# Optimization experiments

Measured on AMD Instinct MI355X. Metric: run time of the kernel, lower is better.

Reference implementation:

```python
import jax, jax.numpy as jnp
import numpy as np

N = 4096
IN_DIM = 512
NUM_HEADS = 8
SUB_DIM = 64
ETA = 0.5
LAMBDA_SPARSE = 0.1
EDGE_PROB = 0.01


def setup_inputs() -> dict:
    key = jax.random.key(0)
    k_h, k_u, k_a = jax.random.split(key, 3)
    H = jax.random.normal(k_h, (N, IN_DIM), dtype=jnp.float32)
    # Per-head orthonormal subspace bases (QR init, as in the torch module)
    raw = jax.random.normal(k_u, (NUM_HEADS, IN_DIM, SUB_DIM), dtype=jnp.float32)
    U = jax.vmap(lambda a: jnp.linalg.qr(a)[0])(raw)  # [K, in_dim, r]
    # Binary adjacency mask with self-loops (float 0/1)
    adj = (jax.random.uniform(k_a, (N, N)) < EDGE_PROB).astype(jnp.float32)
    adj_mask = jnp.maximum(adj, jnp.eye(N, dtype=jnp.float32))
    threshold = jnp.full((IN_DIM,), LAMBDA_SPARSE, dtype=jnp.float32)
    return {"H": H, "adj_mask": adj_mask, "U": U, "threshold": threshold}


def reference(H, adj_mask, U, threshold):
    r = U.shape[-1]
    scale = jnp.asarray(r, H.dtype) ** 0.5
    # Z_k = U_k^T H^T  -> [K, r, n]
    Z = jnp.einsum('kdr,nd->krn', U, H)
    # scores[k, i, j] = Z_k[:, i] . Z_k[:, j] / sqrt(r), masked to neighbors
    scores = jnp.einsum('kri,krj->kij', Z, Z) / scale
    scores = scores + (1.0 - adj_mask) * (-1e9)
    alpha = jax.nn.softmax(scores, axis=-1)          # [K, n, n]
    # Z_agg[k, :, i] = sum_j alpha[k, i, j] * Z_k[:, j]
    Z_agg = jnp.einsum('krj,kij->kri', Z, alpha)      # [K, r, n]
    # project back and sum heads: [n, d]
    agg = jnp.einsum('kdr,kri->id', U, Z_agg)
    H_half = H + ETA * agg
    H_out = jax.nn.relu(H_half - threshold[None, :])
    # orthogonality loss: sum_{k<l} ||U_k^T U_l||_F^2
    gram = jnp.einsum('kdr,lds->klrs', U, U)
    sq = jnp.sum(gram ** 2, axis=(-1, -2))            # [K, K]
    orth_loss = 0.5 * (jnp.sum(sq) - jnp.trace(sq))
    return H_out, orth_loss
```

## Files before the change

### kernel.cpp

```cpp
#include <hip/hip_runtime.h>
#include <hip/hip_bf16.h>

#define NN   4096
#define DD   512
#define KH   8
#define RR   64
#define CAP  128

typedef unsigned short u16;
typedef unsigned int   u32;
typedef __attribute__((ext_vector_type(8))) short short8;
typedef __attribute__((ext_vector_type(4))) float f32x4;

__device__ __forceinline__ float bflo(u32 v){ union{u32 i; float f;} c; c.i = v << 16;        return c.f; }
__device__ __forceinline__ float bfhi(u32 v){ union{u32 i; float f;} c; c.i = v & 0xFFFF0000u; return c.f; }
__device__ __forceinline__ u16 f2bf(float f){ __hip_bfloat16 h = __float2bfloat16(f); return *reinterpret_cast<u16*>(&h); }

__global__ __launch_bounds__(256) void prep_scan(const float* __restrict__ H, const float* __restrict__ U,
                                                 const float* __restrict__ adj,
                                                 u16* __restrict__ Hb, u16* __restrict__ Bt1,
                                                 u16* __restrict__ Bt2,
                                                 int* __restrict__ nlist, int* __restrict__ cnt,
                                                 float* __restrict__ lossA, int* __restrict__ doneA) {
    __shared__ float tile[64][65];
    __shared__ int   list[CAP];
    __shared__ int   cntS;
    const int b = blockIdx.x, t = threadIdx.x;
    if (b < 4096) {
        const int i = b;
        if (t == 0) cntS = 0;
        __syncthreads();
        const float* arow = adj + (size_t)i * NN;
        #pragma unroll
        for (int qq = 0; qq < 4; qq++) {
            int j = (qq * 256 + t) * 4;
            float4 mv = *(const float4*)(arow + j);
            if (mv.x != 0.f) { int p = atomicAdd(&cntS, 1); if (p < CAP) list[p] = j;     }
            if (mv.y != 0.f) { int p = atomicAdd(&cntS, 1); if (p < CAP) list[p] = j + 1; }
            if (mv.z != 0.f) { int p = atomicAdd(&cntS, 1); if (p < CAP) list[p] = j + 2; }
            if (mv.w != 0.f) { int p = atomicAdd(&cntS, 1); if (p < CAP) list[p] = j + 3; }
        }
        __syncthreads();
        const int n = min(cntS, CAP);
        if (t < n) nlist[(size_t)i * CAP + t] = list[t];
        if (t == 0) cnt[i] = n;
        return;
    }
    if (b < 6144) {
        size_t id = (size_t)(b - 4096) * 256 + t;
        float4 v = *(const float4*)(H + id * 4);
        ushort4 o; o.x = f2bf(v.x); o.y = f2bf(v.y); o.z = f2bf(v.z); o.w = f2bf(v.w);
        *(ushort4*)(Hb + id * 4) = o;
        return;
    }
    if (b == 6208) { if (t == 0) { lossA[0] = 0.f; doneA[0] = 0; } return; }
    const int b2 = b - 6144;
    const int k = b2 >> 3, d0 = (b2 & 7) * 64;
    #pragma unroll
    for (int s = 0; s < 4; s++) {
        int u = t + 256 * s;
        int dd = u >> 4, rq = u & 15;
        float4 v = *(const float4*)(U + ((size_t)(k * DD + d0 + dd)) * RR + rq * 4);
        tile[dd][rq * 4 + 0] = v.x; tile[dd][rq * 4 + 1] = v.y;
        tile[dd][rq * 4 + 2] = v.z; tile[dd][rq * 4 + 3] = v.w;
    }
    __syncthreads();
    {   int r = t >> 2;
        #pragma unroll
        for (int ii = 0; ii < 16; ii++) {
            int dd = (t & 3) * 16 + ii;
            Bt1[(size_t)(k * RR + r) * DD + d0 + dd] = f2bf(tile[dd][r]);
        }
    }
    {   int dd = t >> 2, rb = (t & 3) * 16;
        #pragma unroll
        for (int ii = 0; ii < 16; ii++) {
            Bt2[(size_t)(d0 + dd) * DD + k * RR + rb + ii] = f2bf(tile[dd][rb + ii]);
        }
    }
}

__global__ __launch_bounds__(256) void zgemm_mfma(const u16* __restrict__ Hb, const u16* __restrict__ Bt1,
                                                  u16* __restrict__ Zb) {
    __shared__ short As[64][72];
    __shared__ short Bs[64][72];
    const int t = threadIdx.x;
    const int i0 = blockIdx.x * 64, n0 = blockIdx.y * 64;
    const int w = t >> 6, lane = t & 63;
    const int lm = lane & 15, lg = lane >> 4;
    f32x4 acc[4] = {};
    for (int kc = 0; kc < DD; kc += 64) {
        #pragma unroll
        for (int s = 0; s < 2; s++) {
            int c = t + 256 * s; int row = c >> 3, g = c & 7;
            *(short8*)&As[row][g * 8] = *(const short8*)(Hb  + (size_t)(i0 + row) * DD + kc + g * 8);
            *(short8*)&Bs[row][g * 8] = *(const short8*)(Bt1 + (size_t)(n0 + row) * DD + kc + g * 8);
        }
        __syncthreads();
        #pragma unroll
        for (int ks = 0; ks < 64; ks += 32) {
            short8 af = *(const short8*)&As[w * 16 + lm][ks + lg * 8];
            #pragma unroll
            for (int b = 0; b < 4; b++) {
                short8 bfr = *(const short8*)&Bs[b * 16 + lm][ks + lg * 8];
                acc[b] = __builtin_amdgcn_mfma_f32_16x16x32_bf16(af, bfr, acc[b], 0, 0, 0);
            }
        }
        __syncthreads();
    }
    #pragma unroll
    for (int b = 0; b < 4; b++)
        #pragma unroll
        for (int q = 0; q < 4; q++) {
            int row = i0 + w * 16 + lg * 4 + q;
            int col = n0 + b * 16 + lm;
            Zb[(size_t)row * DD + col] = f2bf(acc[b][q]);
        }
}

__global__ __launch_bounds__(512) void attn10(const u16* __restrict__ Zb, const int* __restrict__ nlist,
                                              const int* __restrict__ cnt, u16* __restrict__ Zaggb) {
    const int i = blockIdx.x, t = threadIdx.x;
    const int k = t >> 6, lane = t & 63;
    const int n = lane >> 2, q = lane & 3;
    __shared__ float red[KH][16][68];
    const int ci = cnt[i];
    const int* nl = nlist + (size_t)i * CAP;

    float a[16];
    {
        const uint4* zp = (const uint4*)(Zb + (size_t)i * DD + k * 64 + q * 16);
        uint4 w0 = zp[0], w1 = zp[1];
        a[0] = bflo(w0.x); a[1] = bfhi(w0.x); a[2]  = bflo(w0.y); a[3]  = bfhi(w0.y);
        a[4] = bflo(w0.z); a[5] = bfhi(w0.z); a[6]  = bflo(w0.w); a[7]  = bfhi(w0.w);
        a[8] = bflo(w1.x); a[9] = bfhi(w1.x); a[10] = bflo(w1.y); a[11] = bfhi(w1.y);
        a[12]= bflo(w1.z); a[13]= bfhi(w1.z); a[14] = bflo(w1.w); a[15] = bfhi(w1.w);
    }

    float l = 0.f;
    float acc[16] = {};

    int jCur = nl[(n < ci) ? n : 0];
    const uint4* pp = (const uint4*)(Zb + (size_t)jCur * DD + k * 64 + q * 16);
    uint4 v0 = pp[0], v1 = pp[1];
    int jNext = (16 < ci) ? nl[(16 + n < ci) ? 16 + n : 0] : 0;

    for (int base = 0; base < ci; base += 16) {
        const uint4 c0 = v0, c1 = v1;
        const bool valid = (base + n) < ci;
        if (base + 16 < ci) {
            const uint4* np = (const uint4*)(Zb + (size_t)jNext * DD + k * 64 + q * 16);
            v0 = np[0]; v1 = np[1];
        }
        if (base + 32 < ci)
            jNext = nl[(base + 32 + n < ci) ? base + 32 + n : 0];
        float zf[16];
        zf[0] = bflo(c0.x); zf[1] = bfhi(c0.x); zf[2]  = bflo(c0.y); zf[3]  = bfhi(c0.y);
        zf[4] = bflo(c0.z); zf[5] = bfhi(c0.z); zf[6]  = bflo(c0.w); zf[7]  = bfhi(c0.w);
        zf[8] = bflo(c1.x); zf[9] = bfhi(c1.x); zf[10] = bflo(c1.y); zf[11] = bfhi(c1.y);
        zf[12]= bflo(c1.z); zf[13]= bfhi(c1.z); zf[14] = bflo(c1.w); zf[15] = bfhi(c1.w);
        float s = 0.f;
        #pragma unroll
        for (int d = 0; d < 16; d++) s += zf[d] * a[d];
        s += __shfl_xor(s, 1);
        s += __shfl_xor(s, 2);
        const float e = valid ? __expf(s * 0.125f) : 0.f;
        l += e;
        #pragma unroll
        for (int d = 0; d < 16; d++) acc[d] += e * zf[d];
    }

    #pragma unroll
    for (int off = 4; off < 64; off <<= 1) l += __shfl_xor(l, off);

    float* rp = &red[k][n][q * 16];
    *(float4*)(rp + 0)  = make_float4(acc[0],  acc[1],  acc[2],  acc[3]);
    *(float4*)(rp + 4)  = make_float4(acc[4],  acc[5],  acc[6],  acc[7]);
    *(float4*)(rp + 8)  = make_float4(acc[8],  acc[9],  acc[10], acc[11]);
    *(float4*)(rp + 12) = make_float4(acc[12], acc[13], acc[14], acc[15]);
    __threadfence_block();
    float sum = 0.f;
    #pragma unroll
    for (int nn = 0; nn < 16; nn++) sum += red[k][nn][lane];
    const float outv = sum / l;
    Zaggb[(size_t)i * DD + k * 64 + lane] = f2bf(outv);
}

__global__ __launch_bounds__(256) void outgemm_mfma(const u16* __restrict__ Ab, const u16* __restrict__ Btb,
                                                    const float* __restrict__ H, const float* __restrict__ thr,
                                                    float* __restrict__ out) {
    __shared__ short As[64][72];
    __shared__ short Bs[64][72];
    const int t = threadIdx.x;
    const int i0 = blockIdx.x * 64, n0 = blockIdx.y * 64;
    const int w = t >> 6, lane = t & 63;
    const int lm = lane & 15, lg = lane >> 4;
    f32x4 acc[4] = {};
    for (int kc = 0; kc < DD; kc += 64) {
        #pragma unroll
        for (int s = 0; s < 2; s++) {
            int c = t + 256 * s; int row = c >> 3, g = c & 7;
            *(short8*)&As[row][g * 8] = *(const short8*)(Ab  + (size_t)(i0 + row) * DD + kc + g * 8);
            *(short8*)&Bs[row][g * 8] = *(const short8*)(Btb + (size_t)(n0 + row) * DD + kc + g * 8);
        }
        __syncthreads();
        #pragma unroll
        for (int ks = 0; ks < 64; ks += 32) {
            short8 af = *(const short8*)&As[w * 16 + lm][ks + lg * 8];
            #pragma unroll
            for (int b = 0; b < 4; b++) {
                short8 bfr = *(const short8*)&Bs[b * 16 + lm][ks + lg * 8];
                acc[b] = __builtin_amdgcn_mfma_f32_16x16x32_bf16(af, bfr, acc[b], 0, 0, 0);
            }
        }
        __syncthreads();
    }
    #pragma unroll
    for (int b = 0; b < 4; b++) {
        const int col = n0 + b * 16 + lm;
        const float th = thr[col];
        #pragma unroll
        for (int q = 0; q < 4; q++) {
            int row = i0 + w * 16 + lg * 4 + q;
            float h = H[(size_t)row * DD + col];
            out[(size_t)row * DD + col] = fmaxf(h + 0.5f * acc[b][q] - th, 0.f);
        }
    }
}

__global__ __launch_bounds__(256) void orth_kernel(const float* __restrict__ U, float* __restrict__ loss,
                                                   int* __restrict__ done, float* __restrict__ outLoss) {
    __shared__ float UkT[64][20];
    __shared__ float UlT[64][68];
    const int pb = blockIdx.x >> 2, strip = blockIdx.x & 3;
    int idx = pb, k = 0, lh = 1;
    #pragma unroll
    for (int kk = 0; kk < 8; kk++) {
        int c = 7 - kk;
        if (idx < c) { k = kk; lh = kk + 1 + idx; break; }
        idx -= c;
    }
    const int t = threadIdx.x;
    const int r = t & 15;
    const int s0 = (t >> 4) * 4;
    const int r0g = strip * 16;
    const float* Uk = U + (size_t)k  * DD * RR;
    const float* Ul = U + (size_t)lh * DD * RR;
    float a0 = 0.f, a1 = 0.f, a2 = 0.f, a3 = 0.f;
    for (int dc = 0; dc < DD; dc += 64) {
        {   int dd = t >> 2, rq = t & 3;
            *(float4*)&UkT[dd][rq * 4] = *(const float4*)(Uk + (size_t)(dc + dd) * RR + r0g + rq * 4);
        }
        #pragma unroll
        for (int s = 0; s < 4; s++) {
            int u = t + 256 * s;
            int dd = u >> 4, sq = u & 15;
            *(float4*)&UlT[dd][sq * 4] = *(const float4*)(Ul + (size_t)(dc + dd) * RR + sq * 4);
        }
        __syncthreads();
        #pragma unroll 4
        for (int dd = 0; dd < 64; dd++) {
            float a = UkT[dd][r];
            float4 bv = *(const float4*)&UlT[dd][s0];
            a0 += a * bv.x; a1 += a * bv.y; a2 += a * bv.z; a3 += a * bv.w;
        }
        __syncthreads();
    }
    float v = a0 * a0 + a1 * a1 + a2 * a2 + a3 * a3;
    #pragma unroll
    for (int off = 32; off; off >>= 1) v += __shfl_down(v, off, 64);
    __shared__ float red[4];
    if ((t & 63) == 0) red[t >> 6] = v;
    __syncthreads();
    if (t == 0) {
        atomicAdd(loss, red[0] + red[1] + red[2] + red[3]);
        __threadfence();
        int d = atomicAdd(done, 1);
        if (d == 111) {
            float total = atomicAdd(loss, 0.f);
            outLoss[0] = total;
        }
    }
}

extern "C" void kernel_launch(void* const* d_in, const int* in_sizes, int n_in,
                              void* d_out, int out_size, void* d_ws, size_t ws_size,
                              hipStream_t stream) {
    const float* H   = (const float*)d_in[0];
    const float* adj = (const float*)d_in[1];
    const float* U   = (const float*)d_in[2];
    const float* thr = (const float*)d_in[3];
    float* out = (float*)d_out;

    char* ws = (char*)d_ws;
    float* lossA = (float*)ws;
    int*   doneA = (int*)(ws + 64);
    u16*   Hb    = (u16*)(ws + 1024);
    u16*   Zb    = (u16*)(ws + 1024 + 4u * 1024 * 1024);
    u16*   Zaggb = (u16*)(ws + 1024 + 8u * 1024 * 1024);
    u16*   Bt1   = (u16*)(ws + 1024 + 12u * 1024 * 1024);
    u16*   Bt2   = (u16*)(ws + 1024 + 12u * 1024 * 1024 + 512u * 1024);
    int*   nlist = (int*)(ws + 1024 + 13u * 1024 * 1024);
    int*   cnt   = (int*)(ws + 1024 + 15u * 1024 * 1024 + 512u * 1024);

    prep_scan<<<6209, 256, 0, stream>>>(H, U, adj, Hb, Bt1, Bt2, nlist, cnt, lossA, doneA);
    zgemm_mfma<<<dim3(64, 8), 256, 0, stream>>>(Hb, Bt1, Zb);
    attn10<<<NN, 512, 0, stream>>>(Zb, nlist, cnt, Zaggb);
    outgemm_mfma<<<dim3(64, 8), 256, 0, stream>>>(Zaggb, Bt2, H, thr, out);
    orth_kernel<<<112, 256, 0, stream>>>(U, lossA, doneA, out + (size_t)NN * DD);
}
```

Before: 159.6 us.

## Fold orth loss into prep kernel and remap attention work per neighbor

The orthogonality-loss blocks now run inside the prep kernel and write per-block partial sums, which the output GEMM reduces. This removes a separate launch and the atomic/done-counter handshake. The attention kernel is rewritten so each wavefront handles one neighbor per step across the full 512-wide row, all heads at once. Neighbor indices are staged in shared memory, two neighbors are prefetched ahead, and the per-wave partials are combined through shared memory with a sync. The trade-off is more shared-memory reduction and more inactive work when neighbor counts are uneven.

```diff
diff --git a/kernel.cpp b/kernel.cpp
--- a/kernel.cpp
+++ b/kernel.cpp
@@ -21,28 +21,31 @@
                                                  u16* __restrict__ Hb, u16* __restrict__ Bt1,
                                                  u16* __restrict__ Bt2,
                                                  int* __restrict__ nlist, int* __restrict__ cnt,
-                                                 float* __restrict__ lossA, int* __restrict__ doneA) {
-    __shared__ float tile[64][65];
-    __shared__ int   list[CAP];
-    __shared__ int   cntS;
+                                                 float* __restrict__ lossP) {
+    union SH {
+        struct { float tile[64][65]; int list[CAP]; int cntS; } p;
+        struct { float UkT[64][20]; float UlT[64][68]; } o;
+    };
+    __shared__ SH sh;
+    __shared__ float red4[4];
     const int b = blockIdx.x, t = threadIdx.x;
     if (b < 4096) {
         const int i = b;
-        if (t == 0) cntS = 0;
+        if (t == 0) sh.p.cntS = 0;
         __syncthreads();
         const float* arow = adj + (size_t)i * NN;
         #pragma unroll
         for (int qq = 0; qq < 4; qq++) {
             int j = (qq * 256 + t) * 4;
             float4 mv = *(const float4*)(arow + j);
-            if (mv.x != 0.f) { int p = atomicAdd(&cntS, 1); if (p < CAP) list[p] = j;     }
-            if (mv.y != 0.f) { int p = atomicAdd(&cntS, 1); if (p < CAP) list[p] = j + 1; }
-            if (mv.z != 0.f) { int p = atomicAdd(&cntS, 1); if (p < CAP) list[p] = j + 2; }
-            if (mv.w != 0.f) { int p = atomicAdd(&cntS, 1); if (p < CAP) list[p] = j + 3; }
-        }
-        __syncthreads();
-        const int n = min(cntS, CAP);
-        if (t < n) nlist[(size_t)i * CAP + t] = list[t];
+            if (mv.x != 0.f) { int p = atomicAdd(&sh.p.cntS, 1); if (p < CAP) sh.p.list[p] = j;     }
+            if (mv.y != 0.f) { int p = atomicAdd(&sh.p.cntS, 1); if (p < CAP) sh.p.list[p] = j + 1; }
+            if (mv.z != 0.f) { int p = atomicAdd(&sh.p.cntS, 1); if (p < CAP) sh.p.list[p] = j + 2; }
+            if (mv.w != 0.f) { int p = atomicAdd(&sh.p.cntS, 1); if (p < CAP) sh.p.list[p] = j + 3; }
+        }
+        __syncthreads();
+        const int n = min(sh.p.cntS, CAP);
+        if (t < n) nlist[(size_t)i * CAP + t] = sh.p.list[t];
         if (t == 0) cnt[i] = n;
         return;
     }
@@ -53,31 +56,73 @@
         *(ushort4*)(Hb + id * 4) = o;
         return;
     }
-    if (b == 6208) { if (t == 0) { lossA[0] = 0.f; doneA[0] = 0; } return; }
-    const int b2 = b - 6144;
-    const int k = b2 >> 3, d0 = (b2 & 7) * 64;
-    #pragma unroll
-    for (int s = 0; s < 4; s++) {
-        int u = t + 256 * s;
-        int dd = u >> 4, rq = u & 15;
-        float4 v = *(const float4*)(U + ((size_t)(k * DD + d0 + dd)) * RR + rq * 4);
-        tile[dd][rq * 4 + 0] = v.x; tile[dd][rq * 4 + 1] = v.y;
-        tile[dd][rq * 4 + 2] = v.z; tile[dd][rq * 4 + 3] = v.w;
-    }
+    if (b < 6208) {
+        const int b2 = b - 6144;
+        const int k = b2 >> 3, d0 = (b2 & 7) * 64;
+        #pragma unroll
+        for (int s = 0; s < 4; s++) {
+            int u = t + 256 * s;
+            int dd = u >> 4, rq = u & 15;
+            float4 v = *(const float4*)(U + ((size_t)(k * DD + d0 + dd)) * RR + rq * 4);
+            sh.p.tile[dd][rq * 4 + 0] = v.x; sh.p.tile[dd][rq * 4 + 1] = v.y;
+            sh.p.tile[dd][rq * 4 + 2] = v.z; sh.p.tile[dd][rq * 4 + 3] = v.w;
+        }
+        __syncthreads();
+        {   int r = t >> 2;
+            #pragma unroll
+            for (int ii = 0; ii < 16; ii++) {
+                int dd = (t & 3) * 16 + ii;
+                Bt1[(size_t)(k * RR + r) * DD + d0 + dd] = f2bf(sh.p.tile[dd][r]);
+            }
+        }
+        {   int dd = t >> 2, rb = (t & 3) * 16;
+            #pragma unroll
+            for (int ii = 0; ii < 16; ii++) {
+                Bt2[(size_t)(d0 + dd) * DD + k * RR + rb + ii] = f2bf(sh.p.tile[dd][rb + ii]);
+            }
+        }
+        return;
+    }
+    const int ob = b - 6208;
+    const int pb = ob >> 2, strip = ob & 3;
+    int idx = pb, k = 0, lh = 1;
+    #pragma unroll
+    for (int kk = 0; kk < 8; kk++) {
+        int c = 7 - kk;
+        if (idx < c) { k = kk; lh = kk + 1 + idx; break; }
+        idx -= c;
+    }
+    const int r = t & 15;
+    const int s0 = (t >> 4) * 4;
+    const int r0g = strip * 16;
+    const float* Uk = U + (size_t)k  * DD * RR;
+    const float* Ul = U + (size_t)lh * DD * RR;
+    float a0 = 0.f, a1 = 0.f, a2 = 0.f, a3 = 0.f;
+    for (int dc = 0; dc < DD; dc += 64) {
+        {   int dd = t >> 2, rq = t & 3;
+            *(float4*)&sh.o.UkT[dd][rq * 4] = *(const float4*)(Uk + (size_t)(dc + dd) * RR + r0g + rq * 4);
+        }
+        #pragma unroll
+        for (int s = 0; s < 4; s++) {
+            int u = t + 256 * s;
+            int dd = u >> 4, sq = u & 15;
+            *(float4*)&sh.o.UlT[dd][sq * 4] = *(const float4*)(Ul + (size_t)(dc + dd) * RR + sq * 4);
+        }
+        __syncthreads();
+        #pragma unroll 4
+        for (int dd = 0; dd < 64; dd++) {
+            float a = sh.o.UkT[dd][r];
+            float4 bv = *(const float4*)&sh.o.UlT[dd][s0];
+            a0 += a * bv.x; a1 += a * bv.y; a2 += a * bv.z; a3 += a * bv.w;
+        }
+        __syncthreads();
+    }
+    float v = a0 * a0 + a1 * a1 + a2 * a2 + a3 * a3;
+    #pragma unroll
+    for (int off = 32; off; off >>= 1) v += __shfl_down(v, off, 64);
+    if ((t & 63) == 0) red4[t >> 6] = v;
     __syncthreads();
-    {   int r = t >> 2;
-        #pragma unroll
-        for (int ii = 0; ii < 16; ii++) {
-            int dd = (t & 3) * 16 + ii;
-            Bt1[(size_t)(k * RR + r) * DD + d0 + dd] = f2bf(tile[dd][r]);
-        }
-    }
-    {   int dd = t >> 2, rb = (t & 3) * 16;
-        #pragma unroll
-        for (int ii = 0; ii < 16; ii++) {
-            Bt2[(size_t)(d0 + dd) * DD + k * RR + rb + ii] = f2bf(tile[dd][rb + ii]);
-        }
-    }
+    if (t == 0) lossP[ob] = red4[0] + red4[1] + red4[2] + red4[3];
 }
 
 __global__ __launch_bounds__(256) void zgemm_mfma(const u16* __restrict__ Hb, const u16* __restrict__ Bt1,
@@ -118,81 +163,88 @@
         }
 }
 
-__global__ __launch_bounds__(512) void attn10(const u16* __restrict__ Zb, const int* __restrict__ nlist,
+__global__ __launch_bounds__(512) void attn11(const u16* __restrict__ Zb, const int* __restrict__ nlist,
                                               const int* __restrict__ cnt, u16* __restrict__ Zaggb) {
     const int i = blockIdx.x, t = threadIdx.x;
-    const int k = t >> 6, lane = t & 63;
-    const int n = lane >> 2, q = lane & 3;
-    __shared__ float red[KH][16][68];
+    const int w = t >> 6, lane = t & 63;
+    __shared__ int   nbrS[CAP];
+    __shared__ float red[KH][DD];
+    __shared__ float lS[KH][KH + 1];
     const int ci = cnt[i];
-    const int* nl = nlist + (size_t)i * CAP;
-
-    float a[16];
+    if (t < CAP) nbrS[t] = nlist[(size_t)i * CAP + min(t, ci - 1)];
+    __syncthreads();
+
+    float a[8];
     {
-        const uint4* zp = (const uint4*)(Zb + (size_t)i * DD + k * 64 + q * 16);
-        uint4 w0 = zp[0], w1 = zp[1];
-        a[0] = bflo(w0.x); a[1] = bfhi(w0.x); a[2]  = bflo(w0.y); a[3]  = bfhi(w0.y);
-        a[4] = bflo(w0.z); a[5] = bfhi(w0.z); a[6]  = bflo(w0.w); a[7]  = bfhi(w0.w);
-        a[8] = bflo(w1.x); a[9] = bfhi(w1.x); a[10] = bflo(w1.y); a[11] = bfhi(w1.y);
-        a[12]= bflo(w1.z); a[13]= bfhi(w1.z); a[14] = bflo(w1.w); a[15] = bfhi(w1.w);
+        uint4 av = *(const uint4*)(Zb + (size_t)i * DD + lane * 8);
+        a[0] = bflo(av.x); a[1] = bfhi(av.x); a[2] = bflo(av.y); a[3] = bfhi(av.y);
+        a[4] = bflo(av.z); a[5] = bfhi(av.z); a[6] = bflo(av.w); a[7] = bfhi(av.w);
     }
 
     float l = 0.f;
-    float acc[16] = {};
-
-    int jCur = nl[(n < ci) ? n : 0];
-    const uint4* pp = (const uint4*)(Zb + (size_t)jCur * DD + k * 64 + q * 16);
-    uint4 v0 = pp[0], v1 = pp[1];
-    int jNext = (16 < ci) ? nl[(16 + n < ci) ? 16 + n : 0] : 0;
-
-    for (int base = 0; base < ci; base += 16) {
-        const uint4 c0 = v0, c1 = v1;
-        const bool valid = (base + n) < ci;
-        if (base + 16 < ci) {
-            const uint4* np = (const uint4*)(Zb + (size_t)jNext * DD + k * 64 + q * 16);
-            v0 = np[0]; v1 = np[1];
-        }
-        if (base + 32 < ci)
-            jNext = nl[(base + 32 + n < ci) ? base + 32 + n : 0];
-        float zf[16];
-        zf[0] = bflo(c0.x); zf[1] = bfhi(c0.x); zf[2]  = bflo(c0.y); zf[3]  = bfhi(c0.y);
-        zf[4] = bflo(c0.z); zf[5] = bfhi(c0.z); zf[6]  = bflo(c0.w); zf[7]  = bfhi(c0.w);
-        zf[8] = bflo(c1.x); zf[9] = bfhi(c1.x); zf[10] = bflo(c1.y); zf[11] = bfhi(c1.y);
-        zf[12]= bflo(c1.z); zf[13]= bfhi(c1.z); zf[14] = bflo(c1.w); zf[15] = bfhi(c1.w);
-        float s = 0.f;
-        #pragma unroll
-        for (int d = 0; d < 16; d++) s += zf[d] * a[d];
-        s += __shfl_xor(s, 1);
-        s += __shfl_xor(s, 2);
-        const float e = valid ? __expf(s * 0.125f) : 0.f;
-        l += e;
-        #pragma unroll
-        for (int d = 0; d < 16; d++) acc[d] += e * zf[d];
-    }
-
-    #pragma unroll
-    for (int off = 4; off < 64; off <<= 1) l += __shfl_xor(l, off);
-
-    float* rp = &red[k][n][q * 16];
-    *(float4*)(rp + 0)  = make_float4(acc[0],  acc[1],  acc[2],  acc[3]);
-    *(float4*)(rp + 4)  = make_float4(acc[4],  acc[5],  acc[6],  acc[7]);
-    *(float4*)(rp + 8)  = make_float4(acc[8],  acc[9],  acc[10], acc[11]);
-    *(float4*)(rp + 12) = make_float4(acc[12], acc[13], acc[14], acc[15]);
-    __threadfence_block();
-    float sum = 0.f;
-    #pragma unroll
-    for (int nn = 0; nn < 16; nn++) sum += red[k][nn][lane];
-    const float outv = sum / l;
-    Zaggb[(size_t)i * DD + k * 64 + lane] = f2bf(outv);
+    float acc[8] = {};
+    const int nIt = (ci + 7) >> 3;
+
+    uint4 b0 = *(const uint4*)(Zb + (size_t)nbrS[w] * DD + lane * 8);
+    uint4 b1 = *(const uint4*)(Zb + (size_t)nbrS[min(w + 8, CAP - 1)] * DD + lane * 8);
+
+    #define PROCESS(c, val)                                                        \
+    {   float zf[8];                                                               \
+        zf[0] = bflo(c.x); zf[1] = bfhi(c.x); zf[2] = bflo(c.y); zf[3] = bfhi(c.y);\
+        zf[4] = bflo(c.z); zf[5] = bfhi(c.z); zf[6] = bflo(c.w); zf[7] = bfhi(c.w);\
+        float s = zf[0]*a[0] + zf[1]*a[1] + zf[2]*a[2] + zf[3]*a[3]                \
+                + zf[4]*a[4] + zf[5]*a[5] + zf[6]*a[6] + zf[7]*a[7];               \
+        s += __shfl_xor(s, 1); s += __shfl_xor(s, 2); s += __shfl_xor(s, 4);       \
+        const float e = (val) ? __expf(s * 0.125f) : 0.f;                          \
+        l += e;                                                                    \
+        _Pragma("unroll")                                                          \
+        for (int d = 0; d < 8; d++) acc[d] += e * zf[d];                           \
+    }
+
+    for (int tt = 0; tt < nIt; tt += 2) {
+        {
+            const uint4 c = b0;
+            const int pf = min(w + 8 * (tt + 2), CAP - 1);
+            b0 = *(const uint4*)(Zb + (size_t)nbrS[pf] * DD + lane * 8);
+            const bool val = (w + 8 * tt) < ci;
+            PROCESS(c, val);
+        }
+        if (tt + 1 < nIt) {
+            const uint4 c = b1;
+            const int pf = min(w + 8 * (tt + 3), CAP - 1);
+            b1 = *(const uint4*)(Zb + (size_t)nbrS[pf] * DD + lane * 8);
+            const bool val = (w + 8 * (tt + 1)) < ci;
+            PROCESS(c, val);
+        }
+    }
+    #undef PROCESS
+
+    *(float4*)&red[w][lane * 8]     = make_float4(acc[0], acc[1], acc[2], acc[3]);
+    *(float4*)&red[w][lane * 8 + 4] = make_float4(acc[4], acc[5], acc[6], acc[7]);
+    if ((lane & 7) == 0) lS[w][lane >> 3] = l;
+    __syncthreads();
+
+    const int d = t, k = d >> 6;
+    float ls = 0.f, sum = 0.f;
+    #pragma unroll
+    for (int ww = 0; ww < KH; ww++) { ls += lS[ww][k]; sum += red[ww][d]; }
+    Zaggb[(size_t)i * DD + d] = f2bf(sum / ls);
 }
 
 __global__ __launch_bounds__(256) void outgemm_mfma(const u16* __restrict__ Ab, const u16* __restrict__ Btb,
                                                     const float* __restrict__ H, const float* __restrict__ thr,
+                                                    const float* __restrict__ lossP,
                                                     float* __restrict__ out) {
     __shared__ short As[64][72];
     __shared__ short Bs[64][72];
     const int t = threadIdx.x;
     const int i0 = blockIdx.x * 64, n0 = blockIdx.y * 64;
+    if (i0 == 0 && n0 == 0 && t < 64) {
+        float v = lossP[t] + ((t + 64 < 112) ? lossP[t + 64] : 0.f);
+        #pragma unroll
+        for (int off = 32; off; off >>= 1) v += __shfl_down(v, off, 64);
+        if (t == 0) out[(size_t)NN * DD] = v;
+    }
     const int w = t >> 6, lane = t & 63;
     const int lm = lane & 15, lg = lane >> 4;
     f32x4 acc[4] = {};
@@ -224,61 +276,6 @@
             int row = i0 + w * 16 + lg * 4 + q;
             float h = H[(size_t)row * DD + col];
             out[(size_t)row * DD + col] = fmaxf(h + 0.5f * acc[b][q] - th, 0.f);
-        }
-    }
-}
-
-__global__ __launch_bounds__(256) void orth_kernel(const float* __restrict__ U, float* __restrict__ loss,
-                                                   int* __restrict__ done, float* __restrict__ outLoss) {
-    __shared__ float UkT[64][20];
-    __shared__ float UlT[64][68];
-    const int pb = blockIdx.x >> 2, strip = blockIdx.x & 3;
-    int idx = pb, k = 0, lh = 1;
-    #pragma unroll
-    for (int kk = 0; kk < 8; kk++) {
-        int c = 7 - kk;
-        if (idx < c) { k = kk; lh = kk + 1 + idx; break; }
-        idx -= c;
-    }
-    const int t = threadIdx.x;
-    const int r = t & 15;
-    const int s0 = (t >> 4) * 4;
-    const int r0g = strip * 16;
-    const float* Uk = U + (size_t)k  * DD * RR;
-    const float* Ul = U + (size_t)lh * DD * RR;
-    float a0 = 0.f, a1 = 0.f, a2 = 0.f, a3 = 0.f;
-    for (int dc = 0; dc < DD; dc += 64) {
-        {   int dd = t >> 2, rq = t & 3;
-            *(float4*)&UkT[dd][rq * 4] = *(const float4*)(Uk + (size_t)(dc + dd) * RR + r0g + rq * 4);
-        }
-        #pragma unroll
-        for (int s = 0; s < 4; s++) {
-            int u = t + 256 * s;
-            int dd = u >> 4, sq = u & 15;
-            *(float4*)&UlT[dd][sq * 4] = *(const float4*)(Ul + (size_t)(dc + dd) * RR + sq * 4);
-        }
-        __syncthreads();
-        #pragma unroll 4
-        for (int dd = 0; dd < 64; dd++) {
-            float a = UkT[dd][r];
-            float4 bv = *(const float4*)&UlT[dd][s0];
-            a0 += a * bv.x; a1 += a * bv.y; a2 += a * bv.z; a3 += a * bv.w;
-        }
-        __syncthreads();
-    }
-    float v = a0 * a0 + a1 * a1 + a2 * a2 + a3 * a3;
-    #pragma unroll
-    for (int off = 32; off; off >>= 1) v += __shfl_down(v, off, 64);
-    __shared__ float red[4];
-    if ((t & 63) == 0) red[t >> 6] = v;
-    __syncthreads();
-    if (t == 0) {
-        atomicAdd(loss, red[0] + red[1] + red[2] + red[3]);
-        __threadfence();
-        int d = atomicAdd(done, 1);
-        if (d == 111) {
-            float total = atomicAdd(loss, 0.f);
-            outLoss[0] = total;
         }
     }
 }
@@ -293,8 +290,7 @@
     float* out = (float*)d_out;
 
     char* ws = (char*)d_ws;
-    float* lossA = (float*)ws;
-    int*   doneA = (int*)(ws + 64);
+    float* lossP = (float*)ws;
     u16*   Hb    = (u16*)(ws + 1024);
     u16*   Zb    = (u16*)(ws + 1024 + 4u * 1024 * 1024);
     u16*   Zaggb = (u16*)(ws + 1024 + 8u * 1024 * 1024);
@@ -303,9 +299,8 @@
     int*   nlist = (int*)(ws + 1024 + 13u * 1024 * 1024);
     int*   cnt   = (int*)(ws + 1024 + 15u * 1024 * 1024 + 512u * 1024);
 
-    prep_scan<<<6209, 256, 0, stream>>>(H, U, adj, Hb, Bt1, Bt2, nlist, cnt, lossA, doneA);
+    prep_scan<<<6320, 256, 0, stream>>>(H, U, adj, Hb, Bt1, Bt2, nlist, cnt, lossP);
     zgemm_mfma<<<dim3(64, 8), 256, 0, stream>>>(Hb, Bt1, Zb);
-    attn10<<<NN, 512, 0, stream>>>(Zb, nlist, cnt, Zaggb);
-    outgemm_mfma<<<dim3(64, 8), 256, 0, stream>>>(Zaggb, Bt2, H, thr, out);
-    orth_kernel<<<112, 256, 0, stream>>>(U, lossA, doneA, out + (size_t)NN * DD);
-}
+    attn11<<<NN, 512, 0, stream>>>(Zb, nlist, cnt, Zaggb);
+    outgemm_mfma<<<dim3(64, 8), 256, 0, stream>>>(Zaggb, Bt2, H, thr, lossP, out);
+}
```

New measurement: 173.6 us. 1.09x slower.
